# Optimization experiments

Hardware: AMD Instinct MI355X
Metric: run time of the kernel (lower is better)

Reference implementation:

```python
import jax, jax.numpy as jnp
import numpy as np

SEQ, BATCH, IN_DIM, HID, OUT = 512, 256, 300, 256, 2


def setup_inputs() -> dict:
    key = jax.random.key(0)
    ks = jax.random.split(key, 7)
    s_ih = 1.0 / np.sqrt(HID)
    return {
        "x": jax.random.normal(ks[0], (SEQ, BATCH, IN_DIM), jnp.float32),
        "W_ih": jax.random.uniform(ks[1], (HID, IN_DIM), jnp.float32, -s_ih, s_ih),
        "W_hh": jax.random.uniform(ks[2], (HID, HID), jnp.float32, -s_ih, s_ih),
        "b_ih": jax.random.uniform(ks[3], (HID,), jnp.float32, -s_ih, s_ih),
        "b_hh": jax.random.uniform(ks[4], (HID,), jnp.float32, -s_ih, s_ih),
        "W_fc": jax.random.uniform(ks[5], (OUT, HID), jnp.float32, -s_ih, s_ih),
        "b_fc": jax.random.uniform(ks[6], (OUT,), jnp.float32, -s_ih, s_ih),
    }


def reference(x, W_ih, W_hh, b_ih, b_hh, W_fc, b_fc):
    # Precompute input projection for all timesteps at once: [T, B, H]
    xp = jnp.einsum('tbi,hi->tbh', x, W_ih) + b_ih + b_hh

    def step(h, xt):
        h_new = jnp.tanh(xt + h @ W_hh.T)
        return h_new, None

    h0 = jnp.zeros((x.shape[1], W_hh.shape[0]), x.dtype)
    hT, _ = jax.lax.scan(step, h0, xp)  # hT: [B, H]
    # Dropout(0.3) is identity in eval mode.
    logits = hT @ W_fc.T + b_fc  # [B, 2]
    return jax.nn.log_softmax(logits, axis=-1)
```

## Files before the change

### kernel.cpp

```cpp
#include <hip/hip_runtime.h>
#include <hip/hip_bf16.h>
#include <cstdint>
#include <cstddef>

#define SEQ 512
#define BATCH 256
#define IN_DIM 300
#define HID 256

typedef __attribute__((ext_vector_type(8))) short bf16x8;
typedef __attribute__((ext_vector_type(4))) float f32x4;
typedef __attribute__((ext_vector_type(4))) unsigned int u32x4;

__device__ __forceinline__ unsigned short f2bf(float f) {
  union { float f; unsigned int u; } v; v.f = f;
  unsigned int u = v.u;
  return (unsigned short)((u + 0x7fffu + ((u >> 16) & 1u)) >> 16);
}
__device__ __forceinline__ unsigned short f2bf_fast(float f) {
  union { float f; unsigned int u; } v; v.f = f;
  return (unsigned short)((v.u + 0x8000u) >> 16);
}
__device__ __forceinline__ float bitsf(unsigned int u) {
  union { unsigned int u; float f; } v; v.u = u; return v.f;
}
__device__ __forceinline__ unsigned int cvtpk(float lo, float hi) {
  union { __hip_bfloat162 h; unsigned int u; } c;
  c.h = __float22bfloat162_rn(make_float2(lo, hi));
  return c.u;
}
__device__ __forceinline__ bf16x8 cvt8(float a0,float a1,float a2,float a3,
                                       float a4,float a5,float a6,float a7) {
  union { __hip_bfloat162 h2[4]; bf16x8 v; } c;
  c.h2[0] = __float22bfloat162_rn(make_float2(a0, a1));
  c.h2[1] = __float22bfloat162_rn(make_float2(a2, a3));
  c.h2[2] = __float22bfloat162_rn(make_float2(a4, a5));
  c.h2[3] = __float22bfloat162_rn(make_float2(a6, a7));
  return c.v;
}
__device__ __forceinline__ void barrier_lgkm() {
  asm volatile("s_waitcnt lgkmcnt(0)" ::: "memory");
  __builtin_amdgcn_s_barrier();
  asm volatile("" ::: "memory");
}

__global__ __launch_bounds__(256) void conv_wih(const float* __restrict__ w,
                                                unsigned short* __restrict__ w_bf) {
  int idx = blockIdx.x * 256 + threadIdx.x;
  int n = idx / 320, k = idx - n * 320;
  float v = (k < IN_DIM) ? w[n * IN_DIM + k] : 0.f;
  w_bf[idx] = f2bf(v);
}

__global__ __launch_bounds__(512) void gemm_xp(const float* __restrict__ x,
    const unsigned short* __restrict__ w_bf, const float* __restrict__ b_ih,
    const float* __restrict__ b_hh, unsigned int* __restrict__ xp2)
{
  __shared__ unsigned int a_lds[128][20];
  const int tid  = threadIdx.x;
  const int wave = tid >> 6;
  const int lane = tid & 63;
  const int l15  = lane & 15;
  const int quad = lane >> 4;
  const long m0  = (long)blockIdx.x * 128;

  bf16x8 wf[2][10];
  #pragma unroll
  for (int nt = 0; nt < 2; ++nt) {
    const unsigned short* wp = w_bf + (size_t)(wave*32 + nt*16 + l15) * 320 + quad*8;
    #pragma unroll
    for (int kc = 0; kc < 10; ++kc)
      wf[nt][kc] = *(const bf16x8*)(wp + kc*32);
  }

  f32x4 acc[8][2];
  #pragma unroll
  for (int mt = 0; mt < 8; ++mt) {
    acc[mt][0] = (f32x4){0.f, 0.f, 0.f, 0.f};
    acc[mt][1] = (f32x4){0.f, 0.f, 0.f, 0.f};
  }

  const int ar = tid >> 2;
  const int ac = (tid & 3) * 8;
  const float* xrow = x + (size_t)(m0 + ar) * IN_DIM;

  float av[8];
  {
    float2 p0 = *(const float2*)(xrow + ac + 0);
    float2 p1 = *(const float2*)(xrow + ac + 2);
    float2 p2 = *(const float2*)(xrow + ac + 4);
    float2 p3 = *(const float2*)(xrow + ac + 6);
    av[0]=p0.x; av[1]=p0.y; av[2]=p1.x; av[3]=p1.y;
    av[4]=p2.x; av[5]=p2.y; av[6]=p3.x; av[7]=p3.y;
  }

  #pragma unroll
  for (int kc = 0; kc < 10; ++kc) {
    u32x4 pk;
    pk.x = cvtpk(av[0], av[1]);
    pk.y = cvtpk(av[2], av[3]);
    pk.z = cvtpk(av[4], av[5]);
    pk.w = cvtpk(av[6], av[7]);
    *(u32x4*)&a_lds[ar][(tid & 3) * 4] = pk;
    barrier_lgkm();
    if (kc < 9) {
      const int k0 = (kc + 1) * 32;
      const float* src = xrow + k0 + ac;
      if (k0 + ac + 8 <= IN_DIM) {
        float2 p0 = *(const float2*)(src + 0);
        float2 p1 = *(const float2*)(src + 2);
        float2 p2 = *(const float2*)(src + 4);
        float2 p3 = *(const float2*)(src + 6);
        av[0]=p0.x; av[1]=p0.y; av[2]=p1.x; av[3]=p1.y;
        av[4]=p2.x; av[5]=p2.y; av[6]=p3.x; av[7]=p3.y;
      } else {
        #pragma unroll
        for (int j = 0; j < 8; ++j) av[j] = (k0 + ac + j < IN_DIM) ? src[j] : 0.f;
      }
    }
    #pragma unroll
    for (int mt = 0; mt < 8; ++mt) {
      bf16x8 afr = *(const bf16x8*)&a_lds[mt*16 + l15][quad*4];
      acc[mt][0] = __builtin_amdgcn_mfma_f32_16x16x32_bf16(afr, wf[0][kc], acc[mt][0], 0, 0, 0);
      acc[mt][1] = __builtin_amdgcn_mfma_f32_16x16x32_bf16(afr, wf[1][kc], acc[mt][1], 0, 0, 0);
    }
    barrier_lgkm();
  }

  const int t  = (int)(blockIdx.x >> 1);
  const int b4 = ((int)blockIdx.x & 1) * 32;
  #pragma unroll
  for (int nt = 0; nt < 2; ++nt) {
    const int n = wave*32 + nt*16 + l15;
    const float kb = 2.0f * (b_ih[n] + b_hh[n]);
    const int tid_lo = wave*64 + nt*16 + l15;
    #pragma unroll
    for (int mt = 0; mt < 8; ++mt) {
      const int g = b4 + mt*4 + quad;
      const size_t base = ((size_t)t*64 + g) * 512;
      float y0 = fmaf(2.0f, acc[mt][nt][0], kb);
      float y1 = fmaf(2.0f, acc[mt][nt][1], kb);
      float y2 = fmaf(2.0f, acc[mt][nt][2], kb);
      float y3 = fmaf(2.0f, acc[mt][nt][3], kb);
      xp2[base + tid_lo]      = cvtpk(y0, y1);
      xp2[base + tid_lo + 32] = cvtpk(y2, y3);
    }
  }
}

__global__ __launch_bounds__(512) void rnn_scan(const float* __restrict__ W_hh,
    const unsigned int* __restrict__ xp2, float* __restrict__ hT)
{
  __shared__ alignas(16) unsigned short hbuf[2][4 * 272];
  const int tid  = threadIdx.x;
  const int wave = tid >> 6;
  const int lane = tid & 63;
  const int l15  = lane & 15;
  const int quad = lane >> 4;
  const int g = blockIdx.x;
  const int c0 = wave * 32;

  bf16x8 wf[2][8];
  #pragma unroll
  for (int nt = 0; nt < 2; ++nt) {
    const int n = c0 + nt*16 + l15;
    #pragma unroll
    for (int kc = 0; kc < 8; ++kc) {
      const float* src = W_hh + n*HID + kc*32 + quad*8;
      float4 p0 = *(const float4*)src;
      float4 p1 = *(const float4*)(src + 4);
      wf[nt][kc] = cvt8(p0.x,p0.y,p0.z,p0.w,p1.x,p1.y,p1.z,p1.w);
    }
  }

  const int rb    = (quad >> 1) * 2;
  const int col_e = c0 + (quad & 1) * 16 + l15;
  const int abase = (l15 & 3) * 272 + quad * 8;

  for (int i = tid; i < 4 * 272; i += 512) hbuf[0][i] = 0;

  const unsigned int* xbase = xp2 + (size_t)g * 512 + tid;

  __syncthreads();

  unsigned int xq[16], xqn[16];
  #pragma unroll
  for (int j = 0; j < 16; ++j)
    xq[j] = xbase[(size_t)j * 32768];

  for (int tc = 0; tc < SEQ / 16; ++tc) {
    if (tc < SEQ/16 - 1) {
      const unsigned int* pn = xbase + (size_t)(tc + 1) * 16 * 32768;
      #pragma unroll
      for (int j = 0; j < 16; ++j)
        xqn[j] = pn[(size_t)j * 32768];
    }
    #pragma unroll
    for (int j = 0; j < 16; ++j) {
      const int cur = j & 1;
      bf16x8 afr[8];
      #pragma unroll
      for (int kc = 0; kc < 8; ++kc)
        afr[kc] = *(const bf16x8*)&hbuf[cur][abase + kc*32];
      f32x4 a0A = (f32x4){0.f,0.f,0.f,0.f}, a0B = a0A, a1A = a0A, a1B = a0A;
      #pragma unroll
      for (int kc = 0; kc < 8; kc += 2) {
        a0A = __builtin_amdgcn_mfma_f32_16x16x32_bf16(afr[kc],   wf[0][kc],   a0A, 0, 0, 0);
        a1A = __builtin_amdgcn_mfma_f32_16x16x32_bf16(afr[kc],   wf[1][kc],   a1A, 0, 0, 0);
        a0B = __builtin_amdgcn_mfma_f32_16x16x32_bf16(afr[kc+1], wf[0][kc+1], a0B, 0, 0, 0);
        a1B = __builtin_amdgcn_mfma_f32_16x16x32_bf16(afr[kc+1], wf[1][kc+1], a1B, 0, 0, 0);
      }
      f32x4 acc0 = a0A + a0B;
      f32x4 acc1 = a1A + a1B;
      f32x4 a = (quad & 1) ? acc1 : acc0;
      float s0 = (quad >> 1) ? a[2] : a[0];
      float s1 = (quad >> 1) ? a[3] : a[1];
      float xv0 = bitsf(xq[j] << 16);
      float xv1 = bitsf(xq[j] & 0xffff0000u);
      float y0 = fmaf(2.0f, s0, xv0);
      float y1 = fmaf(2.0f, s1, xv1);
      float h0 = fmaf(-2.0f, __builtin_amdgcn_rcpf(__expf(y0) + 1.0f), 1.0f);
      float h1 = fmaf(-2.0f, __builtin_amdgcn_rcpf(__expf(y1) + 1.0f), 1.0f);
      if (j < 15 || tc < SEQ/16 - 1) {
        hbuf[1 - cur][ rb      * 272 + col_e] = f2bf_fast(h0);
        hbuf[1 - cur][(rb + 1) * 272 + col_e] = f2bf_fast(h1);
      } else {
        hT[(size_t)(g*4 + rb    ) * HID + col_e] = h0;
        hT[(size_t)(g*4 + rb + 1) * HID + col_e] = h1;
      }
      barrier_lgkm();
    }
    if (tc < SEQ/16 - 1) {
      #pragma unroll
      for (int j = 0; j < 16; ++j)
        xq[j] = xqn[j];
    }
  }
}

__global__ __launch_bounds__(64) void fc_head(const float* __restrict__ hT,
    const float* __restrict__ W_fc, const float* __restrict__ b_fc,
    float* __restrict__ out)
{
  const int b = blockIdx.x;
  const int l = threadIdx.x;
  float s0 = 0.f, s1 = 0.f;
  #pragma unroll
  for (int j0 = 0; j0 < HID; j0 += 64) {
    float h = hT[(size_t)b * HID + j0 + l];
    s0 += h * W_fc[j0 + l];
    s1 += h * W_fc[HID + j0 + l];
  }
  #pragma unroll
  for (int off = 32; off > 0; off >>= 1) {
    s0 += __shfl_xor(s0, off, 64);
    s1 += __shfl_xor(s1, off, 64);
  }
  if (l == 0) {
    float l0 = s0 + b_fc[0], l1 = s1 + b_fc[1];
    float m = fmaxf(l0, l1);
    float lse = m + logf(expf(l0 - m) + expf(l1 - m));
    out[b*2 + 0] = l0 - lse;
    out[b*2 + 1] = l1 - lse;
  }
}

extern "C" void kernel_launch(void* const* d_in, const int* in_sizes, int n_in,
                              void* d_out, int out_size, void* d_ws, size_t ws_size,
                              hipStream_t stream) {
  const float* x    = (const float*)d_in[0];
  const float* W_ih = (const float*)d_in[1];
  const float* W_hh = (const float*)d_in[2];
  const float* b_ih = (const float*)d_in[3];
  const float* b_hh = (const float*)d_in[4];
  const float* W_fc = (const float*)d_in[5];
  const float* b_fc = (const float*)d_in[6];
  float* out = (float*)d_out;

  const size_t xp_bytes = (size_t)SEQ * BATCH * HID * 2;
  const size_t wb_bytes = (size_t)256 * 320 * 2;
  const size_t ht_bytes = (size_t)BATCH * HID * 4;
  if (ws_size < xp_bytes + wb_bytes + ht_bytes) return;

  char* ws = (char*)d_ws;
  unsigned int*   xp2  = (unsigned int*)ws;
  unsigned short* w_bf = (unsigned short*)(ws + xp_bytes);
  float*          hT   = (float*)(ws + xp_bytes + wb_bytes);

  hipLaunchKernelGGL(conv_wih, dim3(320),  dim3(256), 0, stream, W_ih, w_bf);
  hipLaunchKernelGGL(gemm_xp,  dim3(1024), dim3(512), 0, stream, x, w_bf, b_ih, b_hh, xp2);
  hipLaunchKernelGGL(rnn_scan, dim3(64),   dim3(512), 0, stream, W_hh, xp2, hT);
  hipLaunchKernelGGL(fc_head,  dim3(BATCH), dim3(64), 0, stream, hT, W_fc, b_fc, out);
}
```

Measured before the change: 492.5 us.

## Double-buffer GEMM LDS tiles, retile W_ih layout, widen scan MFMA chains

The input-projection GEMM now double-buffers its LDS A tile and prefetches x two chunks ahead, which removes one barrier per k-step and gives loads more time to land. The bf16 W_ih conversion writes a fragment-ordered layout so each lane's weight loads are contiguous. In the recurrent scan, the MFMA accumulation is split across four independent accumulator chains instead of two, and the MFMA section is wrapped in s_setprio to shorten the serial per-step dependency latency. Both kernels also gain a launch_bounds occupancy hint of 2, which may force register spills given the large per-thread fragment arrays.

```diff
diff --git a/kernel.cpp b/kernel.cpp
--- a/kernel.cpp
+++ b/kernel.cpp
@@ -44,19 +44,44 @@
   asm volatile("" ::: "memory");
 }
 
+struct F8 { float v[8]; };
+__device__ __forceinline__ F8 load_x8(const float* __restrict__ xrow, int k0, int ac) {
+  F8 r;
+  if (k0 + ac + 8 <= IN_DIM) {
+    float2 p0 = *(const float2*)(xrow + k0 + ac + 0);
+    float2 p1 = *(const float2*)(xrow + k0 + ac + 2);
+    float2 p2 = *(const float2*)(xrow + k0 + ac + 4);
+    float2 p3 = *(const float2*)(xrow + k0 + ac + 6);
+    r.v[0]=p0.x; r.v[1]=p0.y; r.v[2]=p1.x; r.v[3]=p1.y;
+    r.v[4]=p2.x; r.v[5]=p2.y; r.v[6]=p3.x; r.v[7]=p3.y;
+  } else {
+    #pragma unroll
+    for (int j = 0; j < 8; ++j)
+      r.v[j] = (k0 + ac + j < IN_DIM) ? xrow[k0 + ac + j] : 0.f;
+  }
+  return r;
+}
+
 __global__ __launch_bounds__(256) void conv_wih(const float* __restrict__ w,
                                                 unsigned short* __restrict__ w_bf) {
   int idx = blockIdx.x * 256 + threadIdx.x;
-  int n = idx / 320, k = idx - n * 320;
+  int j    = idx & 7;
+  int l15  = (idx >> 3) & 15;
+  int quad = (idx >> 7) & 3;
+  int t    = idx >> 9;
+  int n16  = t / 10;
+  int kc   = t - n16 * 10;
+  int n = n16 * 16 + l15;
+  int k = kc * 32 + quad * 8 + j;
   float v = (k < IN_DIM) ? w[n * IN_DIM + k] : 0.f;
   w_bf[idx] = f2bf(v);
 }
 
-__global__ __launch_bounds__(512) void gemm_xp(const float* __restrict__ x,
+__global__ __launch_bounds__(512, 2) void gemm_xp(const float* __restrict__ x,
     const unsigned short* __restrict__ w_bf, const float* __restrict__ b_ih,
     const float* __restrict__ b_hh, unsigned int* __restrict__ xp2)
 {
-  __shared__ unsigned int a_lds[128][20];
+  __shared__ unsigned int a_lds[2][128][20];
   const int tid  = threadIdx.x;
   const int wave = tid >> 6;
   const int lane = tid & 63;
@@ -67,10 +92,11 @@
   bf16x8 wf[2][10];
   #pragma unroll
   for (int nt = 0; nt < 2; ++nt) {
-    const unsigned short* wp = w_bf + (size_t)(wave*32 + nt*16 + l15) * 320 + quad*8;
+    const unsigned short* wp =
+        w_bf + ((size_t)((wave*2 + nt)*10)*4 + quad)*16*8 + (size_t)l15*8;
     #pragma unroll
     for (int kc = 0; kc < 10; ++kc)
-      wf[nt][kc] = *(const bf16x8*)(wp + kc*32);
+      wf[nt][kc] = *(const bf16x8*)(wp + (size_t)kc*4*16*8);
   }
 
   f32x4 acc[8][2];
@@ -84,45 +110,41 @@
   const int ac = (tid & 3) * 8;
   const float* xrow = x + (size_t)(m0 + ar) * IN_DIM;
 
-  float av[8];
+  F8 av[2];
+  av[0] = load_x8(xrow, 0, ac);
+  av[1] = load_x8(xrow, 32, ac);
   {
-    float2 p0 = *(const float2*)(xrow + ac + 0);
-    float2 p1 = *(const float2*)(xrow + ac + 2);
-    float2 p2 = *(const float2*)(xrow + ac + 4);
-    float2 p3 = *(const float2*)(xrow + ac + 6);
-    av[0]=p0.x; av[1]=p0.y; av[2]=p1.x; av[3]=p1.y;
-    av[4]=p2.x; av[5]=p2.y; av[6]=p3.x; av[7]=p3.y;
-  }
+    u32x4 pk;
+    pk.x = cvtpk(av[0].v[0], av[0].v[1]);
+    pk.y = cvtpk(av[0].v[2], av[0].v[3]);
+    pk.z = cvtpk(av[0].v[4], av[0].v[5]);
+    pk.w = cvtpk(av[0].v[6], av[0].v[7]);
+    *(u32x4*)&a_lds[0][ar][(tid & 3) * 4] = pk;
+  }
+  barrier_lgkm();
 
   #pragma unroll
   for (int kc = 0; kc < 10; ++kc) {
-    u32x4 pk;
-    pk.x = cvtpk(av[0], av[1]);
-    pk.y = cvtpk(av[2], av[3]);
-    pk.z = cvtpk(av[4], av[5]);
-    pk.w = cvtpk(av[6], av[7]);
-    *(u32x4*)&a_lds[ar][(tid & 3) * 4] = pk;
-    barrier_lgkm();
+    const int cur = kc & 1;
+    bf16x8 afr[8];
+    #pragma unroll
+    for (int mt = 0; mt < 8; ++mt)
+      afr[mt] = *(const bf16x8*)&a_lds[cur][mt*16 + l15][quad*4];
     if (kc < 9) {
-      const int k0 = (kc + 1) * 32;
-      const float* src = xrow + k0 + ac;
-      if (k0 + ac + 8 <= IN_DIM) {
-        float2 p0 = *(const float2*)(src + 0);
-        float2 p1 = *(const float2*)(src + 2);
-        float2 p2 = *(const float2*)(src + 4);
-        float2 p3 = *(const float2*)(src + 6);
-        av[0]=p0.x; av[1]=p0.y; av[2]=p1.x; av[3]=p1.y;
-        av[4]=p2.x; av[5]=p2.y; av[6]=p3.x; av[7]=p3.y;
-      } else {
-        #pragma unroll
-        for (int j = 0; j < 8; ++j) av[j] = (k0 + ac + j < IN_DIM) ? src[j] : 0.f;
-      }
-    }
+      const int s = (kc + 1) & 1;
+      u32x4 pk;
+      pk.x = cvtpk(av[s].v[0], av[s].v[1]);
+      pk.y = cvtpk(av[s].v[2], av[s].v[3]);
+      pk.z = cvtpk(av[s].v[4], av[s].v[5]);
+      pk.w = cvtpk(av[s].v[6], av[s].v[7]);
+      *(u32x4*)&a_lds[s][ar][(tid & 3) * 4] = pk;
+    }
+    if (kc < 8)
+      av[kc & 1] = load_x8(xrow, (kc + 2) * 32, ac);
     #pragma unroll
     for (int mt = 0; mt < 8; ++mt) {
-      bf16x8 afr = *(const bf16x8*)&a_lds[mt*16 + l15][quad*4];
-      acc[mt][0] = __builtin_amdgcn_mfma_f32_16x16x32_bf16(afr, wf[0][kc], acc[mt][0], 0, 0, 0);
-      acc[mt][1] = __builtin_amdgcn_mfma_f32_16x16x32_bf16(afr, wf[1][kc], acc[mt][1], 0, 0, 0);
+      acc[mt][0] = __builtin_amdgcn_mfma_f32_16x16x32_bf16(afr[mt], wf[0][kc], acc[mt][0], 0, 0, 0);
+      acc[mt][1] = __builtin_amdgcn_mfma_f32_16x16x32_bf16(afr[mt], wf[1][kc], acc[mt][1], 0, 0, 0);
     }
     barrier_lgkm();
   }
@@ -148,7 +170,7 @@
   }
 }
 
-__global__ __launch_bounds__(512) void rnn_scan(const float* __restrict__ W_hh,
+__global__ __launch_bounds__(512, 2) void rnn_scan(const float* __restrict__ W_hh,
     const unsigned int* __restrict__ xp2, float* __restrict__ hT)
 {
   __shared__ alignas(16) unsigned short hbuf[2][4 * 272];
@@ -202,16 +224,28 @@
       #pragma unroll
       for (int kc = 0; kc < 8; ++kc)
         afr[kc] = *(const bf16x8*)&hbuf[cur][abase + kc*32];
-      f32x4 a0A = (f32x4){0.f,0.f,0.f,0.f}, a0B = a0A, a1A = a0A, a1B = a0A;
-      #pragma unroll
-      for (int kc = 0; kc < 8; kc += 2) {
-        a0A = __builtin_amdgcn_mfma_f32_16x16x32_bf16(afr[kc],   wf[0][kc],   a0A, 0, 0, 0);
-        a1A = __builtin_amdgcn_mfma_f32_16x16x32_bf16(afr[kc],   wf[1][kc],   a1A, 0, 0, 0);
-        a0B = __builtin_amdgcn_mfma_f32_16x16x32_bf16(afr[kc+1], wf[0][kc+1], a0B, 0, 0, 0);
-        a1B = __builtin_amdgcn_mfma_f32_16x16x32_bf16(afr[kc+1], wf[1][kc+1], a1B, 0, 0, 0);
-      }
-      f32x4 acc0 = a0A + a0B;
-      f32x4 acc1 = a1A + a1B;
+      f32x4 a0A = (f32x4){0.f,0.f,0.f,0.f}, a0B = a0A, a0C = a0A, a0D = a0A;
+      f32x4 a1A = a0A, a1B = a0A, a1C = a0A, a1D = a0A;
+      __builtin_amdgcn_s_setprio(1);
+      a0A = __builtin_amdgcn_mfma_f32_16x16x32_bf16(afr[0], wf[0][0], a0A, 0, 0, 0);
+      a1A = __builtin_amdgcn_mfma_f32_16x16x32_bf16(afr[0], wf[1][0], a1A, 0, 0, 0);
+      a0B = __builtin_amdgcn_mfma_f32_16x16x32_bf16(afr[1], wf[0][1], a0B, 0, 0, 0);
+      a1B = __builtin_amdgcn_mfma_f32_16x16x32_bf16(afr[1], wf[1][1], a1B, 0, 0, 0);
+      a0C = __builtin_amdgcn_mfma_f32_16x16x32_bf16(afr[2], wf[0][2], a0C, 0, 0, 0);
+      a1C = __builtin_amdgcn_mfma_f32_16x16x32_bf16(afr[2], wf[1][2], a1C, 0, 0, 0);
+      a0D = __builtin_amdgcn_mfma_f32_16x16x32_bf16(afr[3], wf[0][3], a0D, 0, 0, 0);
+      a1D = __builtin_amdgcn_mfma_f32_16x16x32_bf16(afr[3], wf[1][3], a1D, 0, 0, 0);
+      a0A = __builtin_amdgcn_mfma_f32_16x16x32_bf16(afr[4], wf[0][4], a0A, 0, 0, 0);
+      a1A = __builtin_amdgcn_mfma_f32_16x16x32_bf16(afr[4], wf[1][4], a1A, 0, 0, 0);
+      a0B = __builtin_amdgcn_mfma_f32_16x16x32_bf16(afr[5], wf[0][5], a0B, 0, 0, 0);
+      a1B = __builtin_amdgcn_mfma_f32_16x16x32_bf16(afr[5], wf[1][5], a1B, 0, 0, 0);
+      a0C = __builtin_amdgcn_mfma_f32_16x16x32_bf16(afr[6], wf[0][6], a0C, 0, 0, 0);
+      a1C = __builtin_amdgcn_mfma_f32_16x16x32_bf16(afr[6], wf[1][6], a1C, 0, 0, 0);
+      a0D = __builtin_amdgcn_mfma_f32_16x16x32_bf16(afr[7], wf[0][7], a0D, 0, 0, 0);
+      a1D = __builtin_amdgcn_mfma_f32_16x16x32_bf16(afr[7], wf[1][7], a1D, 0, 0, 0);
+      __builtin_amdgcn_s_setprio(0);
+      f32x4 acc0 = (a0A + a0B) + (a0C + a0D);
+      f32x4 acc1 = (a1A + a1B) + (a1C + a1D);
       f32x4 a = (quad & 1) ? acc1 : acc0;
       float s0 = (quad >> 1) ? a[2] : a[0];
       float s1 = (quad >> 1) ? a[3] : a[1];
```

New measurement: 503.5 us. 1.02x slower.
